# Kernel tuning notes

Hardware: AMD Instinct MI355X
Metric: run time of the kernel (lower is better)

Reference implementation:

```python
import jax, jax.numpy as jnp
import numpy as np

VOXEL_SIZE = jnp.array([0.075, 0.075], dtype=jnp.float32)
PC_RANGE = jnp.array([-54.0, -54.0], dtype=jnp.float32)
FUSION_STRIDE = 8.0
SRC_STRIDES = (4.0, 8.0)
RADII = (2.4, 4.8)
NSAMPLE = 16
NKEY = 500


def _mlp(x, w1, g1, b1, w2, b2):
    # Linear(no bias) + BatchNorm(eval, running mean=0/var=1 -> affine) + ReLU, then Linear
    h = jax.nn.relu((x @ w1) * g1 + b1)
    return h @ w2 + b2


def _world(coords, stride):
    # voxel coord -> world xy center
    return (coords.astype(jnp.float32) + 0.5) * stride * VOXEL_SIZE + PC_RANGE


def _gather_rows(x, idx):
    # x: (B, N, ...), idx: (B, ...) -> per-batch row gather
    return jax.vmap(lambda f, i: f[i])(x, idx)


def _knn(key_world, src_world, src_feat, radius):
    # key_world (B,Nk,2), src_world (B,Ns,2), src_feat (B,Ns,C)
    d2 = jnp.sum((key_world[:, :, None, :] - src_world[:, None, :, :]) ** 2, axis=-1)  # (B,Nk,Ns)
    d2 = jnp.where(d2 <= radius * radius, d2, jnp.inf)
    negd, idx = jax.lax.top_k(-d2, NSAMPLE)  # nearest NSAMPLE within radius, (B,Nk,K)
    valid = jnp.isfinite(negd).astype(src_feat.dtype)  # empty==0 mask
    feats = _gather_rows(src_feat, idx)  # (B,Nk,K,C)
    return feats * valid[..., None]


def setup_inputs() -> dict:
    key = jax.random.key(0)
    ks = jax.random.split(key, 24)
    s = 0.05
    return {
        'fusion_feat': jax.random.normal(ks[0], (2, 20000, 128), jnp.float32),
        'src_feat_a': jax.random.normal(ks[1], (2, 30000, 128), jnp.float32),
        'src_feat_b': jax.random.normal(ks[2], (2, 30000, 128), jnp.float32),
        'heat_w1': jax.random.normal(ks[3], (128, 128), jnp.float32) * s,
        'heat_g1': jnp.ones((128,), jnp.float32),
        'heat_b1': jnp.zeros((128,), jnp.float32),
        'heat_w2': jax.random.normal(ks[4], (128, 10), jnp.float32) * s,
        'heat_b2': jnp.zeros((10,), jnp.float32),
        'knn_w': jax.random.normal(ks[5], (2, 16), jnp.float32) * s,
        'knn_b': jnp.zeros((2,), jnp.float32),
        'kw_w1': jax.random.normal(ks[6], (128, 64), jnp.float32) * s,
        'kw_g1': jnp.ones((64,), jnp.float32),
        'kw_b1': jnp.zeros((64,), jnp.float32),
        'kw_w2': jax.random.normal(ks[7], (64, 3), jnp.float32) * s,
        'kw_b2': jnp.zeros((3,), jnp.float32),
        'fuse_w1': jax.random.normal(ks[8], (256, 256), jnp.float32) * s,
        'fuse_g1': jnp.ones((256,), jnp.float32),
        'fuse_b1': jnp.zeros((256,), jnp.float32),
        'fuse_w2': jax.random.normal(ks[9], (256, 128), jnp.float32) * s,
        'fuse_b2': jnp.zeros((128,), jnp.float32),
        'fusion_coords': jax.random.randint(ks[10], (2, 20000, 2), 0, 180, jnp.int32),
        'src_coords_a': jax.random.randint(ks[11], (2, 30000, 2), 0, 360, jnp.int32),
        'src_coords_b': jax.random.randint(ks[12], (2, 30000, 2), 0, 180, jnp.int32),
    }


def reference(fusion_feat, src_feat_a, src_feat_b, heat_w1, heat_g1, heat_b1,
              heat_w2, heat_b2, knn_w, knn_b, kw_w1, kw_g1, kw_b1, kw_w2, kw_b2,
              fuse_w1, fuse_g1, fuse_b1, fuse_w2, fuse_b2,
              fusion_coords, src_coords_a, src_coords_b):
    B = fusion_feat.shape[0]
    # heatmap head over all fusion voxels
    scores10 = _mlp(fusion_feat, heat_w1, heat_g1, heat_b1, heat_w2, heat_b2)  # (B,Nf,10)
    heat_scores = jnp.max(scores10, axis=-1)
    cls = jnp.argmax(scores10, axis=-1)
    # per-sample top-k key voxel selection
    _, tki = jax.lax.top_k(jax.nn.sigmoid(heat_scores), NKEY)  # (B,Nk)
    key_feat = _gather_rows(fusion_feat, tki)      # (B,Nk,128)
    key_coords = _gather_rows(fusion_coords, tki)  # (B,Nk,2)
    key_class = _gather_rows(cls, tki)             # (B,Nk)
    key_world = _world(key_coords, FUSION_STRIDE)  # (B,Nk,2)

    srcs = ((src_feat_a, src_coords_a), (src_feat_b, src_coords_b))
    mlp_feats = []
    for s, (sf, sc) in enumerate(srcs):
        sw = _world(sc, SRC_STRIDES[s])
        kf = _knn(key_world, sw, sf, RADII[s])  # (B,Nk,K,C), zeroed where empty
        # Linear over the K neighbor axis (knn_feat_mlp: NSAMPLE -> 1)
        mf = jnp.einsum('bnkc,k->bnc', kf, knn_w[s]) + knn_b[s]
        mlp_feats.append(mf)

    w = jax.nn.softmax(_mlp(key_feat, kw_w1, kw_g1, kw_b1, kw_w2, kw_b2), axis=-1)  # (B,Nk,3)
    # faithful to original: key_voxel_feat is re-scaled cumulatively inside the loop
    kvf = key_feat
    fuse_sum = jnp.zeros_like(key_feat)
    for i in range(len(srcs)):
        kvf = w[..., i:i + 1] * kvf
        fuse_sum = fuse_sum + kvf * mlp_feats[i]
    fused = jnp.concatenate([fuse_sum, kvf], axis=-1)  # (B,Nk,256)
    out = _mlp(fused, fuse_w1, fuse_g1, fuse_b1, fuse_w2, fuse_b2)  # (B,Nk,128)

    bs_col = jnp.broadcast_to(jnp.arange(B, dtype=key_coords.dtype)[:, None, None], (B, NKEY, 1))
    key_voxel_indices = jnp.concatenate([bs_col, key_coords], axis=-1).reshape(B * NKEY, 3)
    return (out.reshape(B * NKEY, -1), key_voxel_indices,
            heat_scores.reshape(-1), scores10.reshape(-1, scores10.shape[-1]), key_class)
```

## Files before the change

kernel.cpp:

```cpp
#include <hip/hip_runtime.h>
#include <math.h>

#define BB 2
#define NF 20000
#define NS 30000
#define CH 128
#define NK 500
#define KNN 16
#define KPB 4

#define HA 2.4024f
#define HB 4.8048f
#define NCA 45
#define NCB 23
#define CELLS_A 2025
#define CELLS_B 529
#define TOTPTS (2 * BB * NS)

#define OUT0_OFF 0
#define OUT1_OFF 128000
#define OUT2_OFF 131000
#define OUT3_OFF 171000
#define OUT4_OFF 571000

#define WS_CLS   0
#define WS_TKI   160000
#define WS_KW    164000
#define WS_MF    172000
#define WS_KEYS  WS_MF
#define WS_GSTART 1196000
#define WS_GCUR   1216448
#define WS_PTS    1236880
#define WS_PIDX   2196880

#define CURB(s,b) ((s) ? (4050 + (b) * 529) : ((b) * 2025))
#define STB(s,b)  ((s) ? (4052 + (b) * 530) : ((b) * 2026))

__device__ __forceinline__ unsigned ordf(float s) {
    unsigned u = __float_as_uint(s);
    return (u & 0x80000000u) ? ~u : (u | 0x80000000u);
}

__global__ __launch_bounds__(256) void heat_kernel(
    const float* __restrict__ x,
    const float* __restrict__ w1,
    const float* __restrict__ g1, const float* __restrict__ b1,
    const float* __restrict__ w2,
    const float* __restrict__ b2,
    float* __restrict__ out_heat,
    float* __restrict__ out_s10,
    int* __restrict__ cls,
    unsigned long long* __restrict__ keys)
{
    __shared__ float As[64 * 72];
    __shared__ float Ws[64 * 132];
    __shared__ float W2s[1280];
    const int tid = threadIdx.x;
    const int m0 = blockIdx.x * 64;
    const int tx = tid & 15;
    const int ty = tid >> 4;

    for (int v = tid; v < 1280; v += 256) W2s[v] = w2[v];

    float acc[4][8];
#pragma unroll
    for (int i = 0; i < 4; ++i)
#pragma unroll
        for (int j = 0; j < 8; ++j) acc[i][j] = 0.f;

    const float4* xv = (const float4*)x;
    const float4* w1v = (const float4*)w1;

    for (int kc = 0; kc < 128; kc += 64) {
#pragma unroll
        for (int i = 0; i < 4; ++i) {
            int v = tid + i * 256;
            int row = v >> 4, c4 = v & 15;
            float4 val = xv[(size_t)(m0 + row) * 32 + (kc >> 2) + c4];
            *(float4*)&As[row * 72 + c4 * 4] = val;
        }
#pragma unroll
        for (int i = 0; i < 8; ++i) {
            int v = tid + i * 256;
            int k = v >> 5, c4 = v & 31;
            float4 val = w1v[(size_t)(kc + k) * 32 + c4];
            *(float4*)&Ws[k * 132 + c4 * 4] = val;
        }
        __syncthreads();

        const float* a0p = &As[(ty * 4 + 0) * 72];
        const float* a1p = &As[(ty * 4 + 1) * 72];
        const float* a2p = &As[(ty * 4 + 2) * 72];
        const float* a3p = &As[(ty * 4 + 3) * 72];
#pragma unroll 4
        for (int k = 0; k < 64; ++k) {
            float4 bA = *(const float4*)&Ws[k * 132 + tx * 8];
            float4 bB = *(const float4*)&Ws[k * 132 + tx * 8 + 4];
            float a0 = a0p[k], a1 = a1p[k], a2 = a2p[k], a3 = a3p[k];
            acc[0][0] += a0 * bA.x; acc[0][1] += a0 * bA.y; acc[0][2] += a0 * bA.z; acc[0][3] += a0 * bA.w;
            acc[0][4] += a0 * bB.x; acc[0][5] += a0 * bB.y; acc[0][6] += a0 * bB.z; acc[0][7] += a0 * bB.w;
            acc[1][0] += a1 * bA.x; acc[1][1] += a1 * bA.y; acc[1][2] += a1 * bA.z; acc[1][3] += a1 * bA.w;
            acc[1][4] += a1 * bB.x; acc[1][5] += a1 * bB.y; acc[1][6] += a1 * bB.z; acc[1][7] += a1 * bB.w;
            acc[2][0] += a2 * bA.x; acc[2][1] += a2 * bA.y; acc[2][2] += a2 * bA.z; acc[2][3] += a2 * bA.w;
            acc[2][4] += a2 * bB.x; acc[2][5] += a2 * bB.y; acc[2][6] += a2 * bB.z; acc[2][7] += a2 * bB.w;
            acc[3][0] += a3 * bA.x; acc[3][1] += a3 * bA.y; acc[3][2] += a3 * bA.z; acc[3][3] += a3 * bA.w;
            acc[3][4] += a3 * bB.x; acc[3][5] += a3 * bB.y; acc[3][6] += a3 * bB.z; acc[3][7] += a3 * bB.w;
        }
        __syncthreads();
    }

    float4 g1a = ((const float4*)g1)[tx * 2], g1b = ((const float4*)g1)[tx * 2 + 1];
    float4 b1a = ((const float4*)b1)[tx * 2], b1b = ((const float4*)b1)[tx * 2 + 1];
    float* Hs = Ws;
#pragma unroll
    for (int i = 0; i < 4; ++i) {
        int row = ty * 4 + i;
        float4 hA, hB;
        hA.x = fmaxf(acc[i][0] * g1a.x + b1a.x, 0.f);
        hA.y = fmaxf(acc[i][1] * g1a.y + b1a.y, 0.f);
        hA.z = fmaxf(acc[i][2] * g1a.z + b1a.z, 0.f);
        hA.w = fmaxf(acc[i][3] * g1a.w + b1a.w, 0.f);
        hB.x = fmaxf(acc[i][4] * g1b.x + b1b.x, 0.f);
        hB.y = fmaxf(acc[i][5] * g1b.y + b1b.y, 0.f);
        hB.z = fmaxf(acc[i][6] * g1b.z + b1b.z, 0.f);
        hB.w = fmaxf(acc[i][7] * g1b.w + b1b.w, 0.f);
        *(float4*)&Hs[row * 132 + tx * 8] = hA;
        *(float4*)&Hs[row * 132 + tx * 8 + 4] = hB;
    }
    __syncthreads();

    const int r = tid >> 2;
    const int p = tid & 3;
    float a2[10];
#pragma unroll
    for (int c = 0; c < 10; ++c) a2[c] = 0.f;
    for (int kk = 0; kk < 32; ++kk) {
        int k = kk * 4 + p;
        float hv = Hs[r * 132 + k];
#pragma unroll
        for (int c = 0; c < 10; ++c) a2[c] += hv * W2s[k * 10 + c];
    }
#pragma unroll
    for (int c = 0; c < 10; ++c) {
        a2[c] += __shfl_xor(a2[c], 1);
        a2[c] += __shfl_xor(a2[c], 2);
    }
    if (p == 0) {
        int m = m0 + r;
        float best = -INFINITY;
        int bi = 0;
#pragma unroll
        for (int c = 0; c < 10; ++c) {
            float s = a2[c] + b2[c];
            out_s10[(size_t)m * 10 + c] = s;
            if (s > best) { best = s; bi = c; }
        }
        out_heat[m] = best;
        cls[m] = bi;
        int b = m / NF;
        unsigned i = (unsigned)(m - b * NF);
        float sig = 1.0f / (1.0f + expf(-best));
        keys[m] = ((unsigned long long)ordf(sig) << 32) | (unsigned)(~i);
    }
}

#define H1BINS 16384
#define H2BINS 1024

__global__ __launch_bounds__(1024) void topk_kernel(
    const unsigned long long* __restrict__ keys,
    const int* __restrict__ cls,
    const int* __restrict__ fcoords,
    float* __restrict__ out1,
    float* __restrict__ out4,
    int* __restrict__ tki,
    float* __restrict__ keyworld)
{
    __shared__ unsigned h[H1BINS];
    __shared__ unsigned long long list[1024];
    __shared__ unsigned csum[1024];
    __shared__ unsigned ssum[32];
    __shared__ unsigned sel_s, krem_s, cnt_s;
    const int b = blockIdx.x;
    const int tid = threadIdx.x;
    const unsigned long long* kb = keys + (size_t)b * NF;

    for (int i = tid; i < H1BINS; i += 1024) h[i] = 0u;
    __syncthreads();
#pragma unroll 4
    for (int i = tid; i < NF; i += 1024)
        atomicAdd(&h[(unsigned)(kb[i] >> 50)], 1u);
    __syncthreads();
    {
        unsigned s = 0;
        int base = tid * 16;
#pragma unroll
        for (int j = 0; j < 16; ++j) s += h[base + j];
        csum[tid] = s;
    }
    __syncthreads();
    if (tid < 32) {
        unsigned s = 0;
        for (int j = 0; j < 32; ++j) s += csum[tid * 32 + j];
        ssum[tid] = s;
    }
    __syncthreads();
    if (tid == 0) {
        unsigned K = NK, acc = 0;
        int sidx = 31;
        for (; sidx > 0; --sidx) { if (acc + ssum[sidx] >= K) break; acc += ssum[sidx]; }
        int cidx = sidx * 32 + 31;
        for (;; --cidx) { if (acc + csum[cidx] >= K) break; acc += csum[cidx]; }
        int bin = cidx * 16 + 15;
        for (;; --bin) { if (acc + h[bin] >= K) break; acc += h[bin]; }
        sel_s = (unsigned)bin;
        krem_s = K - acc;
    }
    __syncthreads();
    const unsigned T1 = sel_s;
    const unsigned K2 = krem_s;

    for (int i = tid; i < H2BINS; i += 1024) h[i] = 0u;
    __syncthreads();
#pragma unroll 4
    for (int i = tid; i < NF; i += 1024) {
        unsigned long long key = kb[i];
        if ((unsigned)(key >> 50) == T1)
            atomicAdd(&h[(unsigned)(key >> 40) & 1023u], 1u);
    }
    __syncthreads();
    if (tid < 32) {
        unsigned s = 0;
        for (int j = 0; j < 32; ++j) s += h[tid * 32 + j];
        csum[tid] = s;
    }
    __syncthreads();
    if (tid == 0) {
        unsigned acc = 0;
        int cidx = 31;
        for (; cidx > 0; --cidx) { if (acc + csum[cidx] >= K2) break; acc += csum[cidx]; }
        int bin = cidx * 32 + 31;
        for (;; --bin) { if (acc + h[bin] >= K2) break; acc += h[bin]; }
        sel_s = (T1 << 10) | (unsigned)bin;
        cnt_s = 0u;
    }
    __syncthreads();
    const unsigned thr24 = sel_s;

#pragma unroll 4
    for (int i = tid; i < NF; i += 1024) {
        unsigned long long key = kb[i];
        if ((unsigned)(key >> 40) >= thr24) {
            unsigned pos = atomicAdd(&cnt_s, 1u);
            if (pos < 1024u) list[pos] = key;
        }
    }
    __syncthreads();
    unsigned cc = cnt_s > 1024u ? 1024u : cnt_s;
    if ((unsigned)tid >= cc) list[tid] = 0ull;
    __syncthreads();

    for (int kk = 2; kk <= 1024; kk <<= 1) {
        for (int j = kk >> 1; j > 0; j >>= 1) {
            int i = tid, ixj = i ^ j;
            if (ixj > i) {
                unsigned long long a = list[i], bv = list[ixj];
                bool up = ((i & kk) == 0);
                if (up ? (a < bv) : (a > bv)) { list[i] = bv; list[ixj] = a; }
            }
            __syncthreads();
        }
    }

    if (tid < NK) {
        unsigned long long key = list[tid];
        int idx = (int)(~(unsigned)(key & 0xFFFFFFFFull));
        tki[b * NK + tid] = idx;
        int c0 = fcoords[((size_t)b * NF + idx) * 2 + 0];
        int c1 = fcoords[((size_t)b * NF + idx) * 2 + 1];
        size_t o = (size_t)(b * NK + tid);
        out1[o * 3 + 0] = (float)b;
        out1[o * 3 + 1] = (float)c0;
        out1[o * 3 + 2] = (float)c1;
        float wx = __fadd_rn(__fmul_rn(__fmul_rn(__fadd_rn((float)c0, 0.5f), 8.0f), 0.075f), -54.0f);
        float wy = __fadd_rn(__fmul_rn(__fmul_rn(__fadd_rn((float)c1, 0.5f), 8.0f), 0.075f), -54.0f);
        keyworld[o * 2 + 0] = wx;
        keyworld[o * 2 + 1] = wy;
        out4[o] = (float)cls[(size_t)b * NF + idx];
    }
}

__global__ void grid_zero(int* __restrict__ gcur) {
    int i = blockIdx.x * 1024 + threadIdx.x;
    if (i < 5108) gcur[i] = 0;
}

__device__ __forceinline__ void point_world_cell(
    const int* sca, const int* scb, int g, float& sx, float& sy,
    int& s, int& b, int& i, int& cell)
{
    s = g / (BB * NS);
    int rem = g - s * (BB * NS);
    b = rem / NS;
    i = rem - b * NS;
    const int2* sc = ((const int2*)(s ? scb : sca)) + (size_t)b * NS;
    int2 c = sc[i];
    float stride = s ? 8.0f : 4.0f;
    sx = __fadd_rn(__fmul_rn(__fmul_rn(__fadd_rn((float)c.x, 0.5f), stride), 0.075f), -54.0f);
    sy = __fadd_rn(__fmul_rn(__fmul_rn(__fadd_rn((float)c.y, 0.5f), stride), 0.075f), -54.0f);
    float inv_h = s ? (1.0f / HB) : (1.0f / HA);
    int nc = s ? NCB : NCA;
    int cx = (int)floorf((sx + 54.0f) * inv_h);
    int cy = (int)floorf((sy + 54.0f) * inv_h);
    cx = min(max(cx, 0), nc - 1);
    cy = min(max(cy, 0), nc - 1);
    cell = cy * nc + cx;
}

__global__ __launch_bounds__(256) void grid_count(
    const int* __restrict__ sca, const int* __restrict__ scb,
    int* __restrict__ gcur)
{
    int g = blockIdx.x * 256 + threadIdx.x;
    if (g >= TOTPTS) return;
    float sx, sy; int s, b, i, cell;
    point_world_cell(sca, scb, g, sx, sy, s, b, i, cell);
    atomicAdd(&gcur[CURB(s, b) + cell], 1);
}

__global__ __launch_bounds__(1024) void grid_scan(
    int* __restrict__ gcur, int* __restrict__ gstart)
{
    __shared__ int t0[1024], t1[1024];
    const int sb = blockIdx.x;
    const int s = sb >> 1, b = sb & 1;
    const int n = s ? CELLS_B : CELLS_A;
    const int curb = CURB(s, b);
    const int stb = STB(s, b);
    const int tid = threadIdx.x;
    int i0 = tid * 2, i1 = tid * 2 + 1;
    int c0 = (i0 < n) ? gcur[curb + i0] : 0;
    int c1 = (i1 < n) ? gcur[curb + i1] : 0;
    t0[tid] = c0 + c1;
    __syncthreads();
    int* src = t0; int* dst = t1;
    for (int off = 1; off < 1024; off <<= 1) {
        int v = src[tid];
        if (tid >= off) v += src[tid - off];
        dst[tid] = v;
        __syncthreads();
        int* tmp = src; src = dst; dst = tmp;
    }
    int excl = (tid == 0) ? 0 : src[tid - 1];
    if (i0 < n) { gstart[stb + i0] = excl; gcur[curb + i0] = excl; }
    if (i1 < n) { gstart[stb + i1] = excl + c0; gcur[curb + i1] = excl + c0; }
    if (tid == 0) gstart[stb + n] = NS;
}

__global__ __launch_bounds__(256) void grid_scatter(
    const int* __restrict__ sca, const int* __restrict__ scb,
    int* __restrict__ gcur, float2* __restrict__ pts, int* __restrict__ pidx)
{
    int g = blockIdx.x * 256 + threadIdx.x;
    if (g >= TOTPTS) return;
    float sx, sy; int s, b, i, cell;
    point_world_cell(sca, scb, g, sx, sy, s, b, i, cell);
    int pos = atomicAdd(&gcur[CURB(s, b) + cell], 1);
    size_t base = ((size_t)s * BB + b) * NS;
    pts[base + pos] = make_float2(sx, sy);
    pidx[base + pos] = i;
}

__global__ __launch_bounds__(256) void knn_kernel(
    const float* __restrict__ sfa, const float* __restrict__ sfb,
    const int* __restrict__ gstart,
    const float2* __restrict__ pts, const int* __restrict__ pidx,
    const float* __restrict__ knn_w,
    const float* __restrict__ knn_b,
    const float* __restrict__ keyworld,
    float* __restrict__ mf)
{
    __shared__ unsigned long long list[1024];
    __shared__ unsigned cnt_s;
    const int tid = threadIdx.x;
    const int blk = blockIdx.x;
    const int s = blk / (BB * NK);
    const int rest = blk % (BB * NK);
    const int b = rest / NK;
    const int r = rest % NK;
    const float* sfeat = s ? sfb : sfa;
    const float r2 = s ? (float)(4.8 * 4.8) : (float)(2.4 * 2.4);
    const float inv_h = s ? (1.0f / HB) : (1.0f / HA);
    const int nc = s ? NCB : NCA;
    const int stb = STB(s, b);
    const size_t pbase = ((size_t)s * BB + b) * NS;

    if (tid == 0) cnt_s = 0u;
    __syncthreads();
    const float kx = keyworld[((size_t)b * NK + r) * 2 + 0];
    const float ky = keyworld[((size_t)b * NK + r) * 2 + 1];
    int cx = (int)floorf((kx + 54.0f) * inv_h);
    int cy = (int)floorf((ky + 54.0f) * inv_h);
    cx = min(max(cx, 0), nc - 1);
    cy = min(max(cy, 0), nc - 1);
    const int c0 = max(cx - 1, 0), c1 = min(cx + 1, nc - 1);
    const int cy0 = max(cy - 1, 0), cy1 = min(cy + 1, nc - 1);

    for (int cyy = cy0; cyy <= cy1; ++cyy) {
        int lo = gstart[stb + cyy * nc + c0];
        int hi = gstart[stb + cyy * nc + c1 + 1];
        for (int p = lo + tid; p < hi; p += 256) {
            float2 w = pts[pbase + p];
            float dx = __fsub_rn(kx, w.x);
            float dy = __fsub_rn(ky, w.y);
            float d2 = __fadd_rn(__fmul_rn(dx, dx), __fmul_rn(dy, dy));
            if (d2 <= r2) {
                unsigned pos = atomicAdd(&cnt_s, 1u);
                if (pos < 1024u)
                    list[pos] = ((unsigned long long)__float_as_uint(d2) << 32)
                              | (unsigned)pidx[pbase + p];
            }
        }
    }
    __syncthreads();
    int cc = (int)cnt_s;
    if (cc > 1024) cc = 1024;
    int n2 = 16;
    while (n2 < cc) n2 <<= 1;
    for (int i = tid; i < n2; i += 256)
        if (i >= cc) list[i] = ~0ull;
    __syncthreads();
    for (int kk = 2; kk <= n2; kk <<= 1) {
        for (int j = kk >> 1; j > 0; j >>= 1) {
            for (int i = tid; i < n2; i += 256) {
                int ixj = i ^ j;
                if (ixj > i) {
                    unsigned long long a = list[i], bv = list[ixj];
                    bool up = ((i & kk) == 0);
                    bool sw = up ? (a > bv) : (a < bv);
                    if (sw) { list[i] = bv; list[ixj] = a; }
                }
            }
            __syncthreads();
        }
    }
    if (tid < CH) {
        float acc = knn_b[s];
        int K = cc < KNN ? cc : KNN;
        for (int k = 0; k < K; ++k) {
            unsigned i = (unsigned)(list[k] & 0xFFFFFFFFull);
            acc += knn_w[s * 16 + k] * sfeat[((size_t)b * NS + i) * CH + tid];
        }
        mf[(((size_t)s * BB + b) * NK + r) * CH + tid] = acc;
    }
}

__global__ __launch_bounds__(256) void fuse_kernel(
    const float* __restrict__ ffeat,
    const int* __restrict__ tki,
    const float* __restrict__ kw_w1, const float* __restrict__ kw_g1,
    const float* __restrict__ kw_b1, const float* __restrict__ kw_w2,
    const float* __restrict__ kw_b2,
    const float* __restrict__ fuse_w1, const float* __restrict__ fuse_g1,
    const float* __restrict__ fuse_b1, const float* __restrict__ fuse_w2,
    const float* __restrict__ fuse_b2,
    const float* __restrict__ mf,
    float* __restrict__ out0)
{
    __shared__ float xs[KPB * 128];
    __shared__ float hsX[KPB * 64];
    __shared__ float l3[KPB * 3];
    __shared__ float wsm[KPB * 2];
    __shared__ float fusedv[KPB * 256];
    __shared__ float h2s[KPB * 256];
    __shared__ int idxs[KPB], bs[KPB], rs[KPB];
    const int tid = threadIdx.x;
    const int f0 = blockIdx.x * KPB;

    if (tid < KPB) {
        int flat = f0 + tid;
        int b = flat / NK;
        bs[tid] = b;
        rs[tid] = flat - b * NK;
        idxs[tid] = tki[flat];
    }
    __syncthreads();
    for (int v = tid; v < KPB * 128; v += 256) {
        int key = v >> 7, c = v & 127;
        xs[v] = ffeat[((size_t)bs[key] * NF + idxs[key]) * CH + c];
    }
    __syncthreads();
    if (tid < 64) {
        float h[KPB] = {0.f, 0.f, 0.f, 0.f};
        for (int k = 0; k < 128; ++k) {
            float wv = kw_w1[k * 64 + tid];
#pragma unroll
            for (int j = 0; j < KPB; ++j) h[j] += xs[j * 128 + k] * wv;
        }
        float g = kw_g1[tid], bb = kw_b1[tid];
#pragma unroll
        for (int j = 0; j < KPB; ++j) {
            float t = h[j] * g + bb;
            hsX[j * 64 + tid] = t > 0.f ? t : 0.f;
        }
    }
    __syncthreads();
    if (tid < KPB * 3) {
        int key = tid / 3, jj = tid - key * 3;
        float l = 0.f;
        for (int k = 0; k < 64; ++k) l += hsX[key * 64 + k] * kw_w2[k * 3 + jj];
        l3[key * 3 + jj] = l + kw_b2[jj];
    }
    __syncthreads();
    if (tid < KPB) {
        float l0 = l3[tid * 3], l1 = l3[tid * 3 + 1], l2 = l3[tid * 3 + 2];
        float m = fmaxf(l0, fmaxf(l1, l2));
        float e0 = expf(l0 - m), e1 = expf(l1 - m), e2 = expf(l2 - m);
        float sum = e0 + e1 + e2;
        wsm[tid * 2 + 0] = e0 / sum;
        wsm[tid * 2 + 1] = e1 / sum;
    }
    __syncthreads();
    for (int v = tid; v < KPB * 256; v += 256) {
        int key = v >> 8, c = v & 255;
        float w0 = wsm[key * 2], w1_ = wsm[key * 2 + 1];
        if (c < 128) {
            int b = bs[key], r = rs[key];
            float xv_ = xs[key * 128 + c];
            float m0 = mf[(((size_t)0 * BB + b) * NK + r) * CH + c];
            float m1 = mf[(((size_t)1 * BB + b) * NK + r) * CH + c];
            float kv = w0 * xv_;
            float fs = kv * m0;
            float kv2 = w1_ * kv;
            fusedv[v] = fs + kv2 * m1;
        } else {
            float xv_ = xs[key * 128 + (c - 128)];
            float kv = w0 * xv_;
            fusedv[v] = w1_ * kv;
        }
    }
    __syncthreads();
    {
        float acc4[KPB] = {0.f, 0.f, 0.f, 0.f};
        for (int k = 0; k < 256; ++k) {
            float wv = fuse_w1[k * 256 + tid];
#pragma unroll
            for (int j = 0; j < KPB; ++j) acc4[j] += fusedv[j * 256 + k] * wv;
        }
        float g = fuse_g1[tid], bb = fuse_b1[tid];
#pragma unroll
        for (int j = 0; j < KPB; ++j) {
            float t = acc4[j] * g + bb;
            h2s[j * 256 + tid] = t > 0.f ? t : 0.f;
        }
    }
    __syncthreads();
    if (tid < 128) {
        float o[KPB];
        float bb = fuse_b2[tid];
#pragma unroll
        for (int j = 0; j < KPB; ++j) o[j] = bb;
        for (int k = 0; k < 256; ++k) {
            float wv = fuse_w2[k * 128 + tid];
#pragma unroll
            for (int j = 0; j < KPB; ++j) o[j] += h2s[j * 256 + k] * wv;
        }
#pragma unroll
        for (int j = 0; j < KPB; ++j)
            out0[((size_t)bs[j] * NK + rs[j]) * CH + tid] = o[j];
    }
}

extern "C" void kernel_launch(void* const* d_in, const int* in_sizes, int n_in,
                              void* d_out, int out_size, void* d_ws, size_t ws_size,
                              hipStream_t stream)
{
    const float* fusion_feat = (const float*)d_in[0];
    const float* src_feat_a  = (const float*)d_in[1];
    const float* src_feat_b  = (const float*)d_in[2];
    const float* heat_w1 = (const float*)d_in[3];
    const float* heat_g1 = (const float*)d_in[4];
    const float* heat_b1 = (const float*)d_in[5];
    const float* heat_w2 = (const float*)d_in[6];
    const float* heat_b2 = (const float*)d_in[7];
    const float* knn_w   = (const float*)d_in[8];
    const float* knn_b   = (const float*)d_in[9];
    const float* kw_w1   = (const float*)d_in[10];
    const float* kw_g1   = (const float*)d_in[11];
    const float* kw_b1   = (const float*)d_in[12];
    const float* kw_w2   = (const float*)d_in[13];
    const float* kw_b2   = (const float*)d_in[14];
    const float* fuse_w1 = (const float*)d_in[15];
    const float* fuse_g1 = (const float*)d_in[16];
    const float* fuse_b1 = (const float*)d_in[17];
    const float* fuse_w2 = (const float*)d_in[18];
    const float* fuse_b2 = (const float*)d_in[19];
    const int* fusion_coords = (const int*)d_in[20];
    const int* src_coords_a  = (const int*)d_in[21];
    const int* src_coords_b  = (const int*)d_in[22];

    float* out = (float*)d_out;
    char* ws = (char*)d_ws;
    int* cls = (int*)(ws + WS_CLS);
    int* tki = (int*)(ws + WS_TKI);
    float* keyworld = (float*)(ws + WS_KW);
    float* mf = (float*)(ws + WS_MF);
    unsigned long long* keys = (unsigned long long*)(ws + WS_KEYS);
    int* gstart = (int*)(ws + WS_GSTART);
    int* gcur = (int*)(ws + WS_GCUR);
    float2* pts = (float2*)(ws + WS_PTS);
    int* pidx = (int*)(ws + WS_PIDX);

    heat_kernel<<<(BB * NF) / 64, 256, 0, stream>>>(
        fusion_feat, heat_w1, heat_g1, heat_b1, heat_w2, heat_b2,
        out + OUT2_OFF, out + OUT3_OFF, cls, keys);

    topk_kernel<<<BB, 1024, 0, stream>>>(
        keys, cls, fusion_coords,
        out + OUT1_OFF, out + OUT4_OFF, tki, keyworld);

    grid_zero<<<5, 1024, 0, stream>>>(gcur);
    grid_count<<<(TOTPTS + 255) / 256, 256, 0, stream>>>(src_coords_a, src_coords_b, gcur);
    grid_scan<<<4, 1024, 0, stream>>>(gcur, gstart);
    grid_scatter<<<(TOTPTS + 255) / 256, 256, 0, stream>>>(src_coords_a, src_coords_b, gcur, pts, pidx);

    knn_kernel<<<2 * BB * NK, 256, 0, stream>>>(
        src_feat_a, src_feat_b, gstart, pts, pidx,
        knn_w, knn_b, keyworld, mf);

    fuse_kernel<<<(BB * NK) / KPB, 256, 0, stream>>>(
        fusion_feat, tki, kw_w1, kw_g1, kw_b1, kw_w2, kw_b2,
        fuse_w1, fuse_g1, fuse_b1, fuse_w2, fuse_b2, mf, out + OUT0_OFF);
}
```

Before: 272.4 us.

## Split-K the fuse and KNN reductions across more threads, fold grid zeroing into topk

The grid_zero launch is removed and its zeroing of the cell counters moves into the topk kernel, saving one launch. The KNN feature reduction now uses all 256 threads, with two halves of the neighbor axis combined through shared memory. The fuse kernel moves to 1024 threads per block and splits every matmul over K segments with shared-memory partial sums, so each thread runs a shorter serial loop. The cost is more shared memory and extra barriers in each block.

```diff
diff --git a/kernel.cpp b/kernel.cpp
--- a/kernel.cpp
+++ b/kernel.cpp
@@ -33,6 +33,7 @@
 #define WS_PTS    1236880
 #define WS_PIDX   2196880
 
+#define NGCUR 5108
 #define CURB(s,b) ((s) ? (4050 + (b) * 529) : ((b) * 2025))
 #define STB(s,b)  ((s) ? (4052 + (b) * 530) : ((b) * 2026))
 
@@ -174,7 +175,8 @@
     float* __restrict__ out1,
     float* __restrict__ out4,
     int* __restrict__ tki,
-    float* __restrict__ keyworld)
+    float* __restrict__ keyworld,
+    int* __restrict__ gcur)
 {
     __shared__ unsigned h[H1BINS];
     __shared__ unsigned long long list[1024];
@@ -184,6 +186,9 @@
     const int b = blockIdx.x;
     const int tid = threadIdx.x;
     const unsigned long long* kb = keys + (size_t)b * NF;
+
+    for (int i = b * (NGCUR / 2) + tid; i < (b + 1) * (NGCUR / 2) + (b ? NGCUR & 1 : 0); i += 1024)
+        if (i < NGCUR) gcur[i] = 0;
 
     for (int i = tid; i < H1BINS; i += 1024) h[i] = 0u;
     __syncthreads();
@@ -288,11 +293,6 @@
         keyworld[o * 2 + 1] = wy;
         out4[o] = (float)cls[(size_t)b * NF + idx];
     }
-}
-
-__global__ void grid_zero(int* __restrict__ gcur) {
-    int i = blockIdx.x * 1024 + threadIdx.x;
-    if (i < 5108) gcur[i] = 0;
 }
 
 __device__ __forceinline__ void point_world_cell(
@@ -381,6 +381,7 @@
     float* __restrict__ mf)
 {
     __shared__ unsigned long long list[1024];
+    __shared__ float psum[128];
     __shared__ unsigned cnt_s;
     const int tid = threadIdx.x;
     const int blk = blockIdx.x;
@@ -444,18 +445,23 @@
             __syncthreads();
         }
     }
-    if (tid < CH) {
-        float acc = knn_b[s];
+    {
         int K = cc < KNN ? cc : KNN;
-        for (int k = 0; k < K; ++k) {
+        int col = tid & 127, half = tid >> 7;
+        float acc = 0.f;
+        int k0 = half * 8, k1 = min(K, half * 8 + 8);
+        for (int k = k0; k < k1; ++k) {
             unsigned i = (unsigned)(list[k] & 0xFFFFFFFFull);
-            acc += knn_w[s * 16 + k] * sfeat[((size_t)b * NS + i) * CH + tid];
-        }
-        mf[(((size_t)s * BB + b) * NK + r) * CH + tid] = acc;
-    }
-}
-
-__global__ __launch_bounds__(256) void fuse_kernel(
+            acc += knn_w[s * 16 + k] * sfeat[((size_t)b * NS + i) * CH + col];
+        }
+        if (half) psum[col] = acc;
+        __syncthreads();
+        if (!half)
+            mf[(((size_t)s * BB + b) * NK + r) * CH + col] = knn_b[s] + acc + psum[col];
+    }
+}
+
+__global__ __launch_bounds__(1024) void fuse_kernel(
     const float* __restrict__ ffeat,
     const int* __restrict__ tki,
     const float* __restrict__ kw_w1, const float* __restrict__ kw_g1,
@@ -468,10 +474,13 @@
     float* __restrict__ out0)
 {
     __shared__ float xs[KPB * 128];
+    __shared__ float pkw[4 * KPB * 64];
     __shared__ float hsX[KPB * 64];
+    __shared__ float p2[KPB * 3 * 8];
     __shared__ float l3[KPB * 3];
     __shared__ float wsm[KPB * 2];
     __shared__ float fusedv[KPB * 256];
+    __shared__ float pL[4096];
     __shared__ float h2s[KPB * 256];
     __shared__ int idxs[KPB], bs[KPB], rs[KPB];
     const int tid = threadIdx.x;
@@ -485,31 +494,49 @@
         idxs[tid] = tki[flat];
     }
     __syncthreads();
-    for (int v = tid; v < KPB * 128; v += 256) {
-        int key = v >> 7, c = v & 127;
-        xs[v] = ffeat[((size_t)bs[key] * NF + idxs[key]) * CH + c];
-    }
-    __syncthreads();
-    if (tid < 64) {
-        float h[KPB] = {0.f, 0.f, 0.f, 0.f};
-        for (int k = 0; k < 128; ++k) {
-            float wv = kw_w1[k * 64 + tid];
-#pragma unroll
-            for (int j = 0; j < KPB; ++j) h[j] += xs[j * 128 + k] * wv;
-        }
-        float g = kw_g1[tid], bb = kw_b1[tid];
-#pragma unroll
-        for (int j = 0; j < KPB; ++j) {
-            float t = h[j] * g + bb;
-            hsX[j * 64 + tid] = t > 0.f ? t : 0.f;
-        }
+    if (tid < KPB * 128) {
+        int key = tid >> 7, c = tid & 127;
+        xs[tid] = ffeat[((size_t)bs[key] * NF + idxs[key]) * CH + c];
+    }
+    __syncthreads();
+
+    {
+        int out = tid & 63, key = (tid >> 6) & 3, seg = tid >> 8;
+        float acc = 0.f;
+#pragma unroll 8
+        for (int m = 0; m < 32; ++m) {
+            int k = seg * 32 + m;
+            acc += xs[key * 128 + k] * kw_w1[k * 64 + out];
+        }
+        pkw[(seg * KPB + key) * 64 + out] = acc;
+    }
+    __syncthreads();
+    if (tid < KPB * 64) {
+        int key = tid >> 6, out = tid & 63;
+        float s = pkw[(0 * KPB + key) * 64 + out] + pkw[(1 * KPB + key) * 64 + out]
+                + pkw[(2 * KPB + key) * 64 + out] + pkw[(3 * KPB + key) * 64 + out];
+        float t = s * kw_g1[out] + kw_b1[out];
+        hsX[key * 64 + out] = t > 0.f ? t : 0.f;
+    }
+    __syncthreads();
+
+    if (tid < KPB * 24) {
+        int key = tid / 24, rr = tid % 24, out = rr >> 3, seg = rr & 7;
+        float acc = 0.f;
+#pragma unroll
+        for (int m = 0; m < 8; ++m) {
+            int k = seg * 8 + m;
+            acc += hsX[key * 64 + k] * kw_w2[k * 3 + out];
+        }
+        p2[(key * 3 + out) * 8 + seg] = acc;
     }
     __syncthreads();
     if (tid < KPB * 3) {
-        int key = tid / 3, jj = tid - key * 3;
-        float l = 0.f;
-        for (int k = 0; k < 64; ++k) l += hsX[key * 64 + k] * kw_w2[k * 3 + jj];
-        l3[key * 3 + jj] = l + kw_b2[jj];
+        int key = tid / 3, out = tid % 3;
+        float s = 0.f;
+#pragma unroll
+        for (int j = 0; j < 8; ++j) s += p2[(key * 3 + out) * 8 + j];
+        l3[key * 3 + out] = s + kw_b2[out];
     }
     __syncthreads();
     if (tid < KPB) {
@@ -521,8 +548,9 @@
         wsm[tid * 2 + 1] = e1 / sum;
     }
     __syncthreads();
-    for (int v = tid; v < KPB * 256; v += 256) {
-        int key = v >> 8, c = v & 255;
+
+    {
+        int key = tid >> 8, c = tid & 255;
         float w0 = wsm[key * 2], w1_ = wsm[key * 2 + 1];
         if (c < 128) {
             int b = bs[key], r = rs[key];
@@ -532,42 +560,66 @@
             float kv = w0 * xv_;
             float fs = kv * m0;
             float kv2 = w1_ * kv;
-            fusedv[v] = fs + kv2 * m1;
+            fusedv[tid] = fs + kv2 * m1;
         } else {
             float xv_ = xs[key * 128 + (c - 128)];
             float kv = w0 * xv_;
-            fusedv[v] = w1_ * kv;
-        }
-    }
-    __syncthreads();
+            fusedv[tid] = w1_ * kv;
+        }
+    }
+    __syncthreads();
+
     {
-        float acc4[KPB] = {0.f, 0.f, 0.f, 0.f};
-        for (int k = 0; k < 256; ++k) {
-            float wv = fuse_w1[k * 256 + tid];
-#pragma unroll
-            for (int j = 0; j < KPB; ++j) acc4[j] += fusedv[j * 256 + k] * wv;
-        }
-        float g = fuse_g1[tid], bb = fuse_b1[tid];
-#pragma unroll
-        for (int j = 0; j < KPB; ++j) {
-            float t = acc4[j] * g + bb;
-            h2s[j * 256 + tid] = t > 0.f ? t : 0.f;
-        }
-    }
-    __syncthreads();
-    if (tid < 128) {
-        float o[KPB];
-        float bb = fuse_b2[tid];
-#pragma unroll
-        for (int j = 0; j < KPB; ++j) o[j] = bb;
-        for (int k = 0; k < 256; ++k) {
-            float wv = fuse_w2[k * 128 + tid];
-#pragma unroll
-            for (int j = 0; j < KPB; ++j) o[j] += h2s[j * 256 + k] * wv;
-        }
-#pragma unroll
-        for (int j = 0; j < KPB; ++j)
-            out0[((size_t)bs[j] * NK + rs[j]) * CH + tid] = o[j];
+        int out = tid & 255, seg = tid >> 8;
+        float acc0 = 0.f, acc1 = 0.f, acc2 = 0.f, acc3 = 0.f;
+#pragma unroll 8
+        for (int m = 0; m < 64; ++m) {
+            int k = seg * 64 + m;
+            float wv = fuse_w1[k * 256 + out];
+            acc0 += fusedv[0 * 256 + k] * wv;
+            acc1 += fusedv[1 * 256 + k] * wv;
+            acc2 += fusedv[2 * 256 + k] * wv;
+            acc3 += fusedv[3 * 256 + k] * wv;
+        }
+        pL[(seg * KPB + 0) * 256 + out] = acc0;
+        pL[(seg * KPB + 1) * 256 + out] = acc1;
+        pL[(seg * KPB + 2) * 256 + out] = acc2;
+        pL[(seg * KPB + 3) * 256 + out] = acc3;
+    }
+    __syncthreads();
+    {
+        int key = tid >> 8, out = tid & 255;
+        float s = pL[(0 * KPB + key) * 256 + out] + pL[(1 * KPB + key) * 256 + out]
+                + pL[(2 * KPB + key) * 256 + out] + pL[(3 * KPB + key) * 256 + out];
+        float t = s * fuse_g1[out] + fuse_b1[out];
+        h2s[key * 256 + out] = t > 0.f ? t : 0.f;
+    }
+    __syncthreads();
+
+    {
+        int out = tid & 127, seg = tid >> 7;
+        float acc0 = 0.f, acc1 = 0.f, acc2 = 0.f, acc3 = 0.f;
+#pragma unroll 8
+        for (int m = 0; m < 32; ++m) {
+            int k = seg * 32 + m;
+            float wv = fuse_w2[k * 128 + out];
+            acc0 += h2s[0 * 256 + k] * wv;
+            acc1 += h2s[1 * 256 + k] * wv;
+            acc2 += h2s[2 * 256 + k] * wv;
+            acc3 += h2s[3 * 256 + k] * wv;
+        }
+        pL[(seg * KPB + 0) * 128 + out] = acc0;
+        pL[(seg * KPB + 1) * 128 + out] = acc1;
+        pL[(seg * KPB + 2) * 128 + out] = acc2;
+        pL[(seg * KPB + 3) * 128 + out] = acc3;
+    }
+    __syncthreads();
+    if (tid < KPB * 128) {
+        int key = tid >> 7, out = tid & 127;
+        float s = fuse_b2[out];
+#pragma unroll
+        for (int j = 0; j < 8; ++j) s += pL[(j * KPB + key) * 128 + out];
+        out0[((size_t)bs[key] * NK + rs[key]) * CH + out] = s;
     }
 }
 
@@ -617,9 +669,8 @@
 
     topk_kernel<<<BB, 1024, 0, stream>>>(
         keys, cls, fusion_coords,
-        out + OUT1_OFF, out + OUT4_OFF, tki, keyworld);
-
-    grid_zero<<<5, 1024, 0, stream>>>(gcur);
+        out + OUT1_OFF, out + OUT4_OFF, tki, keyworld, gcur);
+
     grid_count<<<(TOTPTS + 255) / 256, 256, 0, stream>>>(src_coords_a, src_coords_b, gcur);
     grid_scan<<<4, 1024, 0, stream>>>(gcur, gstart);
     grid_scatter<<<(TOTPTS + 255) / 256, 256, 0, stream>>>(src_coords_a, src_coords_b, gcur, pts, pidx);
@@ -628,7 +679,7 @@
         src_feat_a, src_feat_b, gstart, pts, pidx,
         knn_w, knn_b, keyworld, mf);
 
-    fuse_kernel<<<(BB * NK) / KPB, 256, 0, stream>>>(
+    fuse_kernel<<<(BB * NK) / KPB, 1024, 0, stream>>>(
         fusion_feat, tki, kw_w1, kw_g1, kw_b1, kw_w2, kw_b2,
         fuse_w1, fuse_g1, fuse_b1, fuse_w2, fuse_b2, mf, out + OUT0_OFF);
 }
```

New measurement: 273.6 us. Within noise of the previous version (+0.5%).
